# Optimization experiments

Hardware: AMD Instinct MI355X
Metric: run time of the kernel (lower is better)

## Reference

```python
import jax, jax.numpy as jnp
import numpy as np

B, CIN, COUT, M1, M2, H, W = 8, 64, 64, 32, 32, 256, 256
SCALE = 1.0 / (CIN * COUT * 1000)


def setup_inputs() -> dict:
    key = jax.random.key(0)
    ks = jax.random.split(key, 9)
    x = jax.random.normal(ks[0], (B, CIN, H, W), dtype=jnp.float32)
    wshape = (CIN, COUT, M1, M2)
    def w(k):
        return SCALE * jax.random.uniform(k, wshape, dtype=jnp.float32)
    return {
        'x': x,
        'w1r': w(ks[1]), 'w1i': w(ks[2]),
        'w2r': w(ks[3]), 'w2i': w(ks[4]),
        'w3r': w(ks[5]), 'w3i': w(ks[6]),
        'w4r': w(ks[7]), 'w4i': w(ks[8]),
    }


def _compl_mul2d(a, w):
    # (b, i, x, y) x (i, o, x, y) -> (b, o, x, y), complex
    return jnp.einsum('bixy,ioxy->boxy', a, w)


def reference(x, w1r, w1i, w2r, w2i, w3r, w3i, w4r, w4i):
    w1 = w1r + 1j * w1i
    w2 = w2r + 1j * w2i
    w3 = w3r + 1j * w3i
    w4 = w4r + 1j * w4i
    b, _, h, wd = x.shape
    cout = w1.shape[1]
    m1, m2 = w1.shape[2], w1.shape[3]

    x_ft_x = jnp.fft.rfft2(x)                      # (b, cin, h, w//2+1)
    x_ft_z = jnp.fft.rfft2(jnp.swapaxes(x, 2, 3))  # transposed branch

    spec_shape = (b, cout, h, wd // 2 + 1)
    out_ft_x = jnp.zeros(spec_shape, dtype=jnp.complex64)
    out_ft_x = out_ft_x.at[:, :, :m1, :m2].set(_compl_mul2d(x_ft_x[:, :, :m1, :m2], w1))
    out_ft_x = out_ft_x.at[:, :, -m1:, :m2].set(_compl_mul2d(x_ft_x[:, :, -m1:, :m2], w2))

    out_ft_z = jnp.zeros(spec_shape, dtype=jnp.complex64)
    out_ft_z = out_ft_z.at[:, :, :m1, :m2].set(_compl_mul2d(x_ft_z[:, :, :m1, :m2], w3))
    out_ft_z = out_ft_z.at[:, :, -m1:, :m2].set(_compl_mul2d(x_ft_z[:, :, -m1:, :m2], w4))

    out_x = jnp.fft.irfft2(out_ft_x, s=(h, wd))
    out_z = jnp.fft.irfft2(out_ft_z, s=(h, wd))
    return (out_x, out_z)
```

## Files before the change

### kernel.cpp

```cpp
#include <hip/hip_runtime.h>


#define PI_D 3.14159265358979323846

__global__ void tab_init(float* __restrict__ ws) {
  int t = blockIdx.x * blockDim.x + threadIdx.x;
  float* TA = ws;
  float* TB = ws + 16384;
  float* TD = ws + 16384 + 65536;
  float* TE = ws + 16384 + 2 * 65536;
  const double w0 = 2.0 * PI_D / 256.0;
  if (t < 16384) {
    int n = t >> 6, c = t & 63, k = c >> 1, s = c & 1;
    int m = (n * k) & 255;
    double sv, cv; sincos(w0 * m, &sv, &cv);
    TA[t] = (float)(s ? -sv : cv);
  }
  {
    int r = t >> 7, c = t & 127;
    int h = r >> 1, ti = r & 1, j = c >> 1, s = c & 1;
    int kx = (j < 32) ? j : 192 + j;
    int m = (kx * h) & 255;
    double sv, cv; sincos(w0 * m, &sv, &cv);
    TB[t] = (float)((ti == s) ? cv : (ti ? sv : -sv));
  }
  {
    int r = t >> 9, c = t & 511;
    int j = r >> 1, ti = r & 1, h = c >> 1, s = c & 1;
    int kx = (j < 32) ? j : 192 + j;
    int m = (kx * h) & 255;
    double sv, cv; sincos(w0 * m, &sv, &cv);
    TD[t] = (float)((ti == s) ? cv : (ti ? -sv : sv));
  }
  if (t < 16384) {
    int r = t >> 8, w = t & 255, k = r >> 1, s = r & 1;
    int m = (k * w) & 255;
    double sv, cv; sincos(w0 * m, &sv, &cv);
    double amp = (k == 0 ? 1.0 : 2.0) / 65536.0;
    TE[t] = (float)(s ? -amp * sv : amp * cv);
  }
}

template <int BM, int BN, int TM, bool KCONTIG>
__global__ __launch_bounds__((BM / TM) * (BN / 8)) void gemm_t(
    const float* __restrict__ in, const float* __restrict__ tab,
    float* __restrict__ out, int K, int N, int rdiv, int rmul1, int rmul2,
    int sH, int sT, long inStride, long outStride) {
  constexpr int NT = (BM / TM) * (BN / 8);
  constexpr int BK = 32;
  constexpr int CW = BN / 64;
  __shared__ float As[BK][BM + 4];
  __shared__ float Bs[BK][BN + 4];
  const int tid = threadIdx.x;
  const int wave = tid >> 6, lane = tid & 63;
  const int tx = (wave % CW) * 8 + (lane & 7);
  const int ty = (wave / CW) * 8 + (lane >> 3);
  const long bm = (long)blockIdx.x * BM;
  const int bn = blockIdx.y * BN;
  in += (long)blockIdx.z * inStride;
  out += (long)blockIdx.z * outStride;
  float acc[TM][8] = {};

  long abase = 0;
  int am;
  if (KCONTIG) {
    am = tid >> 3;
  } else {
    am = tid % BM;
    int row = (int)bm + am;
    abase = (long)(row / rdiv) * rmul1 + (long)(row % rdiv) * rmul2;
  }

  for (int kt = 0; kt < K; kt += BK) {
    if (KCONTIG) {
      int k4 = (tid & 7) * 4;
      #pragma unroll
      for (int mm = am; mm < BM; mm += NT / 8) {
        const float4 v = *reinterpret_cast<const float4*>(
            in + (bm + mm) * (long)rmul1 + kt + k4);
        As[k4 + 0][mm] = v.x;
        As[k4 + 1][mm] = v.y;
        As[k4 + 2][mm] = v.z;
        As[k4 + 3][mm] = v.w;
      }
    } else {
      #pragma unroll
      for (int k = tid / BM; k < BK; k += (NT / BM)) {
        int kg = kt + k;
        As[k][am] = in[abase + (long)(kg >> 1) * sH + (long)(kg & 1) * sT];
      }
    }
    {
      int n4 = (tid % (BN / 4)) * 4;
      #pragma unroll
      for (int k = tid / (BN / 4); k < BK; k += (NT / (BN / 4))) {
        const float4 v = *reinterpret_cast<const float4*>(
            tab + (long)(kt + k) * N + bn + n4);
        Bs[k][n4 + 0] = v.x;
        Bs[k][n4 + 1] = v.y;
        Bs[k][n4 + 2] = v.z;
        Bs[k][n4 + 3] = v.w;
      }
    }
    __syncthreads();
    #pragma unroll
    for (int k = 0; k < BK; ++k) {
      float a[TM], b[8];
      const float4* ap = reinterpret_cast<const float4*>(&As[k][ty * TM]);
      #pragma unroll
      for (int i = 0; i < TM / 4; ++i) {
        float4 v = ap[i];
        a[i * 4 + 0] = v.x; a[i * 4 + 1] = v.y;
        a[i * 4 + 2] = v.z; a[i * 4 + 3] = v.w;
      }
      const float4* bp = reinterpret_cast<const float4*>(&Bs[k][tx * 8]);
      {
        float4 v0 = bp[0], v1 = bp[1];
        b[0] = v0.x; b[1] = v0.y; b[2] = v0.z; b[3] = v0.w;
        b[4] = v1.x; b[5] = v1.y; b[6] = v1.z; b[7] = v1.w;
      }
      #pragma unroll
      for (int i = 0; i < TM; ++i)
        #pragma unroll
        for (int j = 0; j < 8; ++j) acc[i][j] = fmaf(a[i], b[j], acc[i][j]);
    }
    __syncthreads();
  }

  #pragma unroll
  for (int i = 0; i < TM; ++i) {
    long row = bm + ty * TM + i;
    float4 v0 = make_float4(acc[i][0], acc[i][1], acc[i][2], acc[i][3]);
    float4 v1 = make_float4(acc[i][4], acc[i][5], acc[i][6], acc[i][7]);
    float* p = out + row * (long)N + bn + tx * 8;
    *reinterpret_cast<float4*>(p) = v0;
    *reinterpret_cast<float4*>(p + 4) = v1;
  }
}

__global__ __launch_bounds__(512) void modemix(
    const float* __restrict__ Bbuf, float* __restrict__ Cbuf,
    const float* __restrict__ w1r, const float* __restrict__ w1i,
    const float* __restrict__ w2r, const float* __restrict__ w2i,
    const float* __restrict__ w3r, const float* __restrict__ w3i,
    const float* __restrict__ w4r, const float* __restrict__ w4i) {
  __shared__ float2 Bin[8 * 32 * 16];
  const int tid = threadIdx.x;
  const int j = blockIdx.x;
  const int kyh = blockIdx.y;
  const int br = blockIdx.z;
  const float* wr;
  const float* wi;
  int kx;
  if (j < 32) {
    kx = j;
    wr = br ? w3r : w1r;
    wi = br ? w3i : w1i;
  } else {
    kx = j - 32;
    wr = br ? w4r : w2r;
    wi = br ? w4i : w2i;
  }
  const float* Bb = Bbuf + (long)br * 2097152;
  float* Cb = Cbuf + (long)br * 2097152;
  const int kyl = tid & 15;
  const int og = tid >> 4;
  const int o0 = og * 2;
  const int ky = kyh * 16 + kyl;
  float accr[8][2] = {}, acci[8][2] = {};

  for (int ic = 0; ic < 2; ++ic) {
    __syncthreads();
    #pragma unroll
    for (int p = 0; p < 8; ++p) {
      int u = tid + p * 512;
      int ukyl = u & 15;
      int uii = (u >> 4) & 31;
      int ub = u >> 9;
      int i = ic * 32 + uii;
      int uky = kyh * 16 + ukyl;
      const float* src = Bb + ((long)((ub * 64 + i) * 32 + uky)) * 128 + 2 * j;
      Bin[(ub * 32 + uii) * 16 + ukyl] = *reinterpret_cast<const float2*>(src);
    }
    __syncthreads();
    for (int ii = 0; ii < 32; ++ii) {
      int i = ic * 32 + ii;
      long wbase = ((long)(i * 64 + o0) * 32 + kx) * 32 + ky;
      float wr0 = wr[wbase], wi0 = wi[wbase];
      float wr1 = wr[wbase + 1024], wi1 = wi[wbase + 1024];
      #pragma unroll
      for (int b = 0; b < 8; ++b) {
        float2 v = Bin[(b * 32 + ii) * 16 + kyl];
        accr[b][0] = fmaf(v.x, wr0, fmaf(-v.y, wi0, accr[b][0]));
        acci[b][0] = fmaf(v.x, wi0, fmaf(v.y, wr0, acci[b][0]));
        accr[b][1] = fmaf(v.x, wr1, fmaf(-v.y, wi1, accr[b][1]));
        acci[b][1] = fmaf(v.x, wi1, fmaf(v.y, wr1, acci[b][1]));
      }
    }
  }
  #pragma unroll
  for (int b = 0; b < 8; ++b) {
    #pragma unroll
    for (int q = 0; q < 2; ++q) {
      float2 v = make_float2(accr[b][q], acci[b][q]);
      float* dst = Cb + (long)b * 262144 + (long)j * 4096 + (o0 + q) * 64 + ky * 2;
      *reinterpret_cast<float2*>(dst) = v;
    }
  }
}

extern "C" void kernel_launch(void* const* d_in, const int* in_sizes, int n_in,
                              void* d_out, int out_size, void* d_ws,
                              size_t ws_size, hipStream_t stream) {
  const float* x = (const float*)d_in[0];
  const float* w1r = (const float*)d_in[1];
  const float* w1i = (const float*)d_in[2];
  const float* w2r = (const float*)d_in[3];
  const float* w2i = (const float*)d_in[4];
  const float* w3r = (const float*)d_in[5];
  const float* w3i = (const float*)d_in[6];
  const float* w4r = (const float*)d_in[7];
  const float* w4i = (const float*)d_in[8];
  float* ws = (float*)d_ws;

  float* TA = ws;
  float* TB = TA + 16384;
  float* TD = TB + 65536;
  float* TE = TD + 65536;
  float* Abuf = TE + 16384;
  float* Bbuf = Abuf + 16777216;
  float* Cbuf = Bbuf + 4194304;
  float* Dbuf = Abuf;
  float* out = (float*)d_out;

  hipLaunchKernelGGL(tab_init, dim3(256), dim3(256), 0, stream, ws);

  hipLaunchKernelGGL((gemm_t<256, 64, 8, true>), dim3(512, 1, 1), dim3(256), 0,
                     stream, x, TA, Abuf, 256, 64, 1, 256, 0, 2, 1, 0L, 0L);
  hipLaunchKernelGGL((gemm_t<256, 64, 8, false>), dim3(512, 1, 1), dim3(256), 0,
                     stream, x, TA, Abuf + 8388608, 256, 64, 256, 65536, 1, 512,
                     256, 0L, 0L);
  hipLaunchKernelGGL((gemm_t<128, 64, 4, false>), dim3(128, 2, 2), dim3(256), 0,
                     stream, Abuf, TB, Bbuf, 512, 128, 32, 16384, 2, 64, 1,
                     8388608L, 2097152L);
  hipLaunchKernelGGL(modemix, dim3(64, 2, 2), dim3(512), 0, stream, Bbuf, Cbuf,
                     w1r, w1i, w2r, w2i, w3r, w3i, w4r, w4i);
  hipLaunchKernelGGL((gemm_t<128, 128, 8, false>), dim3(128, 4, 2), dim3(256),
                     0, stream, Cbuf, TD, Dbuf, 128, 512, 2048, 262144, 2, 4096,
                     1, 2097152L, 8388608L);
  hipLaunchKernelGGL((gemm_t<128, 128, 8, false>), dim3(1024, 2, 2), dim3(256),
                     0, stream, Dbuf, TE, out, 64, 256, 256, 16384, 2, 512, 1,
                     8388608L, 33554432L);
}
```

Baseline: 941.7 us.

## Use direct global-to-LDS loads and vectorized strided A-tile loads in GEMMs

Splits the GEMM template into three load modes. The strided-input GEMMs now stage A and B tiles with the global_load_lds builtin or with float4 loads that are de-interleaved into LDS. This replaces the earlier per-element scalar gathers. LDS padding is removed for the non-contiguous modes so the direct LDS copies line up, and occupancy hints are added to the launch bounds. Dropping the padding may bring back LDS bank conflicts in the compute loop, and the direct-to-LDS path depends on 16-byte alignment of the strided addresses.

```diff
diff --git a/kernel.cpp b/kernel.cpp
--- a/kernel.cpp
+++ b/kernel.cpp
@@ -41,16 +41,23 @@
   }
 }
 
-template <int BM, int BN, int TM, bool KCONTIG>
-__global__ __launch_bounds__((BM / TM) * (BN / 8)) void gemm_t(
+__device__ __forceinline__ void gl16(const float* g, float* l) {
+  __builtin_amdgcn_global_load_lds(
+      (const __attribute__((address_space(1))) void*)g,
+      (__attribute__((address_space(3))) void*)l, 16, 0, 0);
+}
+
+template <int BM, int BN, int TM, int MODE>
+__global__ __launch_bounds__((BM / TM) * (BN / 8), MODE == 0 ? 4 : 5) void gemm_t(
     const float* __restrict__ in, const float* __restrict__ tab,
     float* __restrict__ out, int K, int N, int rdiv, int rmul1, int rmul2,
     int sH, int sT, long inStride, long outStride) {
   constexpr int NT = (BM / TM) * (BN / 8);
   constexpr int BK = 32;
   constexpr int CW = BN / 64;
-  __shared__ float As[BK][BM + 4];
-  __shared__ float Bs[BK][BN + 4];
+  constexpr int PAD = (MODE == 0) ? 4 : 0;
+  __shared__ float As[BK][BM + PAD];
+  __shared__ float Bs[BK][BN + PAD];
   const int tid = threadIdx.x;
   const int wave = tid >> 6, lane = tid & 63;
   const int tx = (wave % CW) * 8 + (lane & 7);
@@ -62,17 +69,21 @@
   float acc[TM][8] = {};
 
   long abase = 0;
-  int am;
-  if (KCONTIG) {
+  int am = 0;
+  if constexpr (MODE == 0) {
     am = tid >> 3;
-  } else {
-    am = tid % BM;
+  } else if constexpr (MODE == 1) {
+    am = 4 * (tid % (BM / 4));
     int row = (int)bm + am;
     abase = (long)(row / rdiv) * rmul1 + (long)(row % rdiv) * rmul2;
+  } else {
+    am = 2 * (tid % (BM / 2));
+    int row = (int)bm + am;
+    abase = (long)(row / rdiv) * rmul1 + (long)(row % rdiv) * rmul2;
   }
 
   for (int kt = 0; kt < K; kt += BK) {
-    if (KCONTIG) {
+    if constexpr (MODE == 0) {
       int k4 = (tid & 7) * 4;
       #pragma unroll
       for (int mm = am; mm < BM; mm += NT / 8) {
@@ -83,14 +94,26 @@
         As[k4 + 2][mm] = v.z;
         As[k4 + 3][mm] = v.w;
       }
+    } else if constexpr (MODE == 1) {
+      constexpr int KSTEP = NT / (BM / 4);
+      #pragma unroll
+      for (int k = tid / (BM / 4); k < BK; k += KSTEP) {
+        int kg = kt + k;
+        gl16(in + abase + (long)(kg >> 1) * sH + (long)(kg & 1) * sT,
+             &As[k][am]);
+      }
     } else {
-      #pragma unroll
-      for (int k = tid / BM; k < BK; k += (NT / BM)) {
-        int kg = kt + k;
-        As[k][am] = in[abase + (long)(kg >> 1) * sH + (long)(kg & 1) * sT];
-      }
-    }
-    {
+      constexpr int KH = NT / (BM / 2);
+      #pragma unroll
+      for (int i = 0; i < (BK / 2) / KH; ++i) {
+        int khi = tid / (BM / 2) + i * KH;
+        const float4 v = *reinterpret_cast<const float4*>(
+            in + abase + (long)(kt / 2 + khi) * sH);
+        *reinterpret_cast<float2*>(&As[2 * khi][am]) = make_float2(v.x, v.z);
+        *reinterpret_cast<float2*>(&As[2 * khi + 1][am]) = make_float2(v.y, v.w);
+      }
+    }
+    if constexpr (MODE == 0) {
       int n4 = (tid % (BN / 4)) * 4;
       #pragma unroll
       for (int k = tid / (BN / 4); k < BK; k += (NT / (BN / 4))) {
@@ -100,6 +123,12 @@
         Bs[k][n4 + 1] = v.y;
         Bs[k][n4 + 2] = v.z;
         Bs[k][n4 + 3] = v.w;
+      }
+    } else {
+      int n4 = (tid % (BN / 4)) * 4;
+      #pragma unroll
+      for (int k = tid / (BN / 4); k < BK; k += (NT / (BN / 4))) {
+        gl16(tab + (long)(kt + k) * N + bn + n4, &Bs[k][n4]);
       }
     }
     __syncthreads();
@@ -235,20 +264,20 @@
 
   hipLaunchKernelGGL(tab_init, dim3(256), dim3(256), 0, stream, ws);
 
-  hipLaunchKernelGGL((gemm_t<256, 64, 8, true>), dim3(512, 1, 1), dim3(256), 0,
+  hipLaunchKernelGGL((gemm_t<256, 64, 8, 0>), dim3(512, 1, 1), dim3(256), 0,
                      stream, x, TA, Abuf, 256, 64, 1, 256, 0, 2, 1, 0L, 0L);
-  hipLaunchKernelGGL((gemm_t<256, 64, 8, false>), dim3(512, 1, 1), dim3(256), 0,
+  hipLaunchKernelGGL((gemm_t<256, 64, 8, 1>), dim3(512, 1, 1), dim3(256), 0,
                      stream, x, TA, Abuf + 8388608, 256, 64, 256, 65536, 1, 512,
                      256, 0L, 0L);
-  hipLaunchKernelGGL((gemm_t<128, 64, 4, false>), dim3(128, 2, 2), dim3(256), 0,
+  hipLaunchKernelGGL((gemm_t<128, 64, 4, 2>), dim3(128, 2, 2), dim3(256), 0,
                      stream, Abuf, TB, Bbuf, 512, 128, 32, 16384, 2, 64, 1,
                      8388608L, 2097152L);
   hipLaunchKernelGGL(modemix, dim3(64, 2, 2), dim3(512), 0, stream, Bbuf, Cbuf,
                      w1r, w1i, w2r, w2i, w3r, w3i, w4r, w4i);
-  hipLaunchKernelGGL((gemm_t<128, 128, 8, false>), dim3(128, 4, 2), dim3(256),
+  hipLaunchKernelGGL((gemm_t<128, 128, 8, 2>), dim3(128, 4, 2), dim3(256),
                      0, stream, Cbuf, TD, Dbuf, 128, 512, 2048, 262144, 2, 4096,
                      1, 2097152L, 8388608L);
-  hipLaunchKernelGGL((gemm_t<128, 128, 8, false>), dim3(1024, 2, 2), dim3(256),
+  hipLaunchKernelGGL((gemm_t<128, 128, 8, 2>), dim3(1024, 2, 2), dim3(256),
                      0, stream, Dbuf, TE, out, 64, 256, 256, 16384, 2, 512, 1,
                      8388608L, 33554432L);
 }
```

Result: faster. 837.4 us, median of 2 (-11.1%).
